# Performance work log

Measured on AMD Instinct MI355X. Metric: run time of the kernel, lower is better.

## Reference

```python
import math
import jax, jax.numpy as jnp
import numpy as np

B, S, D = 32, 2048, 128

def setup_inputs() -> dict:
    key = jax.random.key(0)
    kq, kk, kv, km = jax.random.split(key, 4)
    q = jax.random.normal(kq, (B, S, D), dtype=jnp.float32)
    k = jax.random.normal(kk, (B, S, D), dtype=jnp.float32)
    v = jax.random.normal(kv, (B, S, D), dtype=jnp.float32)
    mask = jax.random.uniform(km, (B, S, S), dtype=jnp.float32)
    return {"q": q, "k": k, "v": v, "mask": mask}

def reference(q, k, v, mask):
    # scaled_product = (q @ k^T) / sqrt(d), then MULTIPLICATIVE mask, softmax, @ v
    scale = 1.0 / math.sqrt(k.shape[-1])
    scores = jnp.einsum("bqd,bkd->bqk", q, k) * scale  # [B, Sq, Sk]
    scores = scores * mask
    weights = jax.nn.softmax(scores, axis=-1)
    return jnp.einsum("bqk,bkd->bqd", weights, v)
```

## Files before the change

### kernel.cpp

```cpp
#include <hip/hip_runtime.h>
#include <math.h>

#define BATCH 32
#define SEQ   2048
#define DH    128
#define QT    64
#define KT    64
#define SCALE 0.08838834764831845f

typedef _Float16 f16;
typedef _Float16 f16x4 __attribute__((ext_vector_type(4)));
typedef _Float16 f16x8 __attribute__((ext_vector_type(8)));
typedef float    f32x4 __attribute__((ext_vector_type(4)));

__device__ __forceinline__ void gld16(const void* g, void* l) {
    __builtin_amdgcn_global_load_lds(
        (const __attribute__((address_space(1))) unsigned int*)g,
        (__attribute__((address_space(3))) unsigned int*)l,
        16, 0, 0);
}

__global__ __launch_bounds__(256)
void cvt_k_kernel(const float* __restrict__ src, f16* __restrict__ dst) {
    size_t i = ((size_t)blockIdx.x * 256 + threadIdx.x) * 8;
    f32x4 a = *(const f32x4*)&src[i];
    f32x4 c = *(const f32x4*)&src[i + 4];
    f16x8 h = { (f16)a.x,(f16)a.y,(f16)a.z,(f16)a.w,(f16)c.x,(f16)c.y,(f16)c.z,(f16)c.w };
    *(f16x8*)&dst[i] = h;
}

__global__ __launch_bounds__(256)
void tr_v_kernel(const float* __restrict__ v, f16* __restrict__ vt) {
    __shared__ f16 t[128 * 80];
    const int tid  = threadIdx.x;
    const int srow = tid >> 5, scol = tid & 31;
    const int b  = blockIdx.x >> 5;
    const int s0 = (blockIdx.x & 31) * 64;
    const size_t base = (size_t)b * SEQ * DH;
    #pragma unroll
    for (int p = 0; p < 8; ++p) {
        int j = p * 8 + srow;
        const float* vr = &v[base + (size_t)(s0 + j) * DH];
        #pragma unroll
        for (int i = 0; i < 4; ++i)
            t[(scol + 32 * i) * 80 + j] = (f16)vr[scol + 32 * i];
    }
    __syncthreads();
    #pragma unroll
    for (int p = 0; p < 4; ++p) {
        int c = p * 256 + tid;
        int d = c >> 3, col = (c & 7) * 8;
        f16x8 h = *(const f16x8*)&t[d * 80 + col];
        *(f16x8*)&vt[(size_t)b * DH * SEQ + (size_t)d * SEQ + s0 + col] = h;
    }
}

__global__ __launch_bounds__(256, 4)
void ScaledDotProductAttention_46720654246409_kernel(
    const float* __restrict__ q, const f16* __restrict__ k16,
    const f16* __restrict__ vt16, const float* __restrict__ mask,
    float* __restrict__ out)
{
    __shared__ f16 ks[64 * 128];
    __shared__ f16 vs[128 * 64];
    __shared__ f16 ps[4 * 16 * 64];

    const int tid  = threadIdx.x;
    const int wv   = tid >> 6;
    const int lane = tid & 63;
    const int quad = lane >> 4;
    const int l16  = lane & 15;
    const int m3   = l16 & 7;
    const int srow = tid >> 5;
    const int scol = tid & 31;

    const int bidx = blockIdx.x;
    const int b    = bidx >> 5;
    const int q0   = (bidx & 31) * QT;

    const size_t qkvBase = (size_t)b * SEQ * DH;
    const size_t mBase   = (size_t)b * SEQ * SEQ;

    char* ksb = (char*)ks;
    char* vsb = (char*)vs;
    char* psb = (char*)ps + wv * 2048;

    #pragma unroll
    for (int p = 0; p < 8; ++p) {
        int r = p * 8 + srow;
        f32x4 x = *(const f32x4*)&q[qkvBase + (size_t)(q0 + r) * DH + scol * 4];
        f16x4 h = { (f16)x.x, (f16)x.y, (f16)x.z, (f16)x.w };
        *(f16x4*)(ksb + r * 256 + ((scol * 8) ^ ((r & 7) << 4))) = h;
    }
    __syncthreads();

    f16x8 aq[4];
    #pragma unroll
    for (int dc = 0; dc < 4; ++dc)
        aq[dc] = *(const f16x8*)(ksb + (wv * 16 + l16) * 256 + ((dc * 64 + quad * 16) ^ (m3 << 4)));
    __syncthreads();

    float m_run = -INFINITY, l_run = 0.f;
    f32x4 o[8];
    #pragma unroll
    for (int f = 0; f < 8; ++f) o[f] = (f32x4){0.f, 0.f, 0.f, 0.f};

    const f16* kbase = k16  + qkvBase;
    const f16* vbase = vt16 + (size_t)b * DH * SEQ;

    #pragma unroll 1
    for (int kt = 0; kt < SEQ / KT; ++kt) {
        const int k0 = kt * KT;

        #pragma unroll
        for (int i = 0; i < 4; ++i) {
            int c   = wv * 4 + i;
            int row = c * 4 + (lane >> 4);
            gld16(kbase + (size_t)(k0 + row) * DH + 8 * ((lane & 15) ^ (row & 7)),
                  ksb + c * 1024);
        }
        #pragma unroll
        for (int i = 0; i < 4; ++i) {
            int c   = wv * 4 + i;
            int row = c * 8 + (lane >> 3);
            gld16(vbase + (size_t)row * SEQ + k0 + 8 * ((lane & 7) ^ (row & 7)),
                  vsb + c * 1024);
        }

        f32x4 mk[4];
        const float* mrow = &mask[mBase + (size_t)(q0 + wv * 16 + l16) * SEQ + k0 + quad * 4];
        #pragma unroll
        for (int f = 0; f < 4; ++f)
            mk[f] = __builtin_nontemporal_load((const f32x4*)(mrow + f * 16));

        __syncthreads();

        f32x4 sc[4];
        #pragma unroll
        for (int f = 0; f < 4; ++f) {
            sc[f] = (f32x4){0.f, 0.f, 0.f, 0.f};
            #pragma unroll
            for (int dc = 0; dc < 4; ++dc) {
                f16x8 kf = *(const f16x8*)(ksb + (f * 16 + l16) * 256 +
                                           ((dc * 64 + quad * 16) ^ (m3 << 4)));
                sc[f] = __builtin_amdgcn_mfma_f32_16x16x32_f16(kf, aq[dc], sc[f], 0, 0, 0);
            }
        }

        float sf[4][4];
        float mx = -INFINITY;
        #pragma unroll
        for (int f = 0; f < 4; ++f)
            #pragma unroll
            for (int r = 0; r < 4; ++r) {
                sf[f][r] = sc[f][r] * SCALE * mk[f][r];
                mx = fmaxf(mx, sf[f][r]);
            }
        mx = fmaxf(mx, __shfl_xor(mx, 16));
        mx = fmaxf(mx, __shfl_xor(mx, 32));
        float mn = fmaxf(m_run, mx);
        float al = __expf(m_run - mn);
        float sum = 0.f;
        float pv[4][4];
        #pragma unroll
        for (int f = 0; f < 4; ++f)
            #pragma unroll
            for (int r = 0; r < 4; ++r) { pv[f][r] = __expf(sf[f][r] - mn); sum += pv[f][r]; }
        sum += __shfl_xor(sum, 16);
        sum += __shfl_xor(sum, 32);
        m_run = mn;
        l_run = l_run * al + sum;
        float alpha[4];
        #pragma unroll
        for (int r = 0; r < 4; ++r) alpha[r] = __shfl(al, quad * 4 + r, 16);

        #pragma unroll
        for (int f = 0; f < 4; ++f) {
            f16x4 pk = { (f16)pv[f][0], (f16)pv[f][1], (f16)pv[f][2], (f16)pv[f][3] };
            *(f16x4*)(psb + l16 * 128 + ((f * 32 + quad * 8) ^ (m3 << 4))) = pk;
        }
        asm volatile("s_waitcnt lgkmcnt(0)" ::: "memory");

        f16x8 ap0 = *(const f16x8*)(psb + l16 * 128 + ((quad * 16) ^ (m3 << 4)));
        f16x8 ap1 = *(const f16x8*)(psb + l16 * 128 + ((64 + quad * 16) ^ (m3 << 4)));

        #pragma unroll
        for (int f = 0; f < 8; ++f) {
            #pragma unroll
            for (int r = 0; r < 4; ++r) o[f][r] *= alpha[r];
            const char* vrow = vsb + (f * 16 + l16) * 128;
            f16x8 bv0 = *(const f16x8*)(vrow + ((quad * 16) ^ (m3 << 4)));
            f16x8 bv1 = *(const f16x8*)(vrow + ((64 + quad * 16) ^ (m3 << 4)));
            o[f] = __builtin_amdgcn_mfma_f32_16x16x32_f16(ap0, bv0, o[f], 0, 0, 0);
            o[f] = __builtin_amdgcn_mfma_f32_16x16x32_f16(ap1, bv1, o[f], 0, 0, 0);
        }
        __syncthreads();
    }

    float linv[4];
    #pragma unroll
    for (int r = 0; r < 4; ++r) linv[r] = 1.0f / __shfl(l_run, quad * 4 + r, 16);
    #pragma unroll
    for (int r = 0; r < 4; ++r)
        #pragma unroll
        for (int f = 0; f < 8; ++f)
            __builtin_nontemporal_store(o[f][r] * linv[r],
                &out[qkvBase + (size_t)(q0 + wv * 16 + quad * 4 + r) * DH + f * 16 + l16]);
}

__global__ __launch_bounds__(256, 3)
void attn_fallback_kernel(
    const float* __restrict__ q, const float* __restrict__ k,
    const float* __restrict__ v, const float* __restrict__ mask,
    float* __restrict__ out)
{
    __shared__ f16 ks[KT * 136];
    __shared__ f16 vs[DH * 72];
    __shared__ f16 ps[4 * 16 * 72];

    const int tid  = threadIdx.x;
    const int wv   = tid >> 6;
    const int lane = tid & 63;
    const int quad = lane >> 4;
    const int l16  = lane & 15;
    const int srow = tid >> 5;
    const int scol = tid & 31;

    const int bidx = blockIdx.x;
    const int b    = bidx >> 5;
    const int q0   = (bidx & 31) * QT;

    const size_t qkvBase = (size_t)b * SEQ * DH;
    const size_t mBase   = (size_t)b * SEQ * SEQ;

    #pragma unroll
    for (int p = 0; p < 8; ++p) {
        int r = p * 8 + srow;
        f32x4 x = *(const f32x4*)&q[qkvBase + (size_t)(q0 + r) * DH + scol * 4];
        f16x4 h = { (f16)x.x, (f16)x.y, (f16)x.z, (f16)x.w };
        *(f16x4*)&ks[r * 136 + scol * 4] = h;
    }
    __syncthreads();

    f16x8 aq[4];
    #pragma unroll
    for (int dc = 0; dc < 4; ++dc)
        aq[dc] = *(const f16x8*)&ks[(wv * 16 + l16) * 136 + dc * 32 + quad * 8];
    __syncthreads();

    float m_run[4] = { -INFINITY, -INFINITY, -INFINITY, -INFINITY };
    float l_run[4] = { 0.f, 0.f, 0.f, 0.f };
    f32x4 o[8];
    #pragma unroll
    for (int f = 0; f < 8; ++f) o[f] = (f32x4){0.f, 0.f, 0.f, 0.f};

    for (int kt = 0; kt < SEQ / KT; ++kt) {
        const int k0 = kt * KT;

        float mk[4][4];
        #pragma unroll
        for (int f = 0; f < 4; ++f)
            #pragma unroll
            for (int r = 0; r < 4; ++r)
                mk[f][r] = mask[mBase + (size_t)(q0 + wv*16 + quad*4 + r) * SEQ
                                + k0 + f*16 + l16];

        #pragma unroll
        for (int p = 0; p < 8; ++p) {
            int r = p * 8 + srow;
            f32x4 x = *(const f32x4*)&k[qkvBase + (size_t)(k0 + r) * DH + scol * 4];
            f16x4 h = { (f16)x.x, (f16)x.y, (f16)x.z, (f16)x.w };
            *(f16x4*)&ks[r * 136 + scol * 4] = h;
        }
        #pragma unroll
        for (int p = 0; p < 8; ++p) {
            int j = p * 8 + srow;
            const float* vr = &v[qkvBase + (size_t)(k0 + j) * DH];
            #pragma unroll
            for (int i = 0; i < 4; ++i)
                vs[(scol + 32*i) * 72 + j] = (f16)vr[scol + 32*i];
        }
        __syncthreads();

        f32x4 sc[4];
        #pragma unroll
        for (int f = 0; f < 4; ++f) {
            sc[f] = (f32x4){0.f, 0.f, 0.f, 0.f};
            #pragma unroll
            for (int dc = 0; dc < 4; ++dc) {
                f16x8 bk = *(const f16x8*)&ks[(f*16 + l16) * 136 + dc*32 + quad*8];
                sc[f] = __builtin_amdgcn_mfma_f32_16x16x32_f16(aq[dc], bk, sc[f], 0, 0, 0);
            }
        }

        float pj[4][4];
        float alpha[4];
        #pragma unroll
        for (int r = 0; r < 4; ++r) {
            float sf[4];
            #pragma unroll
            for (int f = 0; f < 4; ++f) sf[f] = sc[f][r] * SCALE * mk[f][r];
            float mx = fmaxf(fmaxf(sf[0], sf[1]), fmaxf(sf[2], sf[3]));
            #pragma unroll
            for (int off = 1; off < 16; off <<= 1)
                mx = fmaxf(mx, __shfl_xor(mx, off, 16));
            float mn = fmaxf(m_run[r], mx);
            float al = __expf(m_run[r] - mn);
            float sum = 0.f;
            #pragma unroll
            for (int f = 0; f < 4; ++f) { pj[f][r] = __expf(sf[f] - mn); sum += pj[f][r]; }
            #pragma unroll
            for (int off = 1; off < 16; off <<= 1)
                sum += __shfl_xor(sum, off, 16);
            m_run[r] = mn;
            l_run[r] = l_run[r] * al + sum;
            alpha[r] = al;
        }

        #pragma unroll
        for (int f = 0; f < 4; ++f)
            #pragma unroll
            for (int r = 0; r < 4; ++r)
                ps[(wv*16 + quad*4 + r) * 72 + f*16 + l16] = (f16)pj[f][r];
        asm volatile("s_waitcnt lgkmcnt(0)" ::: "memory");

        f16x8 ap0 = *(const f16x8*)&ps[(wv*16 + l16) * 72 + quad*8];
        f16x8 ap1 = *(const f16x8*)&ps[(wv*16 + l16) * 72 + 32 + quad*8];

        #pragma unroll
        for (int f = 0; f < 8; ++f) {
            #pragma unroll
            for (int r = 0; r < 4; ++r) o[f][r] *= alpha[r];
            f16x8 bv0 = *(const f16x8*)&vs[(f*16 + l16) * 72 + quad*8];
            f16x8 bv1 = *(const f16x8*)&vs[(f*16 + l16) * 72 + 32 + quad*8];
            o[f] = __builtin_amdgcn_mfma_f32_16x16x32_f16(ap0, bv0, o[f], 0, 0, 0);
            o[f] = __builtin_amdgcn_mfma_f32_16x16x32_f16(ap1, bv1, o[f], 0, 0, 0);
        }
        __syncthreads();
    }

    #pragma unroll
    for (int r = 0; r < 4; ++r) {
        float inv = 1.0f / l_run[r];
        #pragma unroll
        for (int f = 0; f < 8; ++f)
            out[qkvBase + (size_t)(q0 + wv*16 + quad*4 + r) * DH + f*16 + l16]
                = o[f][r] * inv;
    }
}

extern "C" void kernel_launch(void* const* d_in, const int* in_sizes, int n_in,
                              void* d_out, int out_size, void* d_ws, size_t ws_size,
                              hipStream_t stream) {
    const float* q    = (const float*)d_in[0];
    const float* k    = (const float*)d_in[1];
    const float* v    = (const float*)d_in[2];
    const float* mask = (const float*)d_in[3];
    float* out = (float*)d_out;

    const size_t elems = (size_t)BATCH * SEQ * DH;
    if (d_ws && ws_size >= 2 * elems * sizeof(f16)) {
        f16* k16  = (f16*)d_ws;
        f16* vt16 = k16 + elems;
        hipLaunchKernelGGL(cvt_k_kernel, dim3((unsigned)(elems / 2048)), dim3(256), 0, stream,
                           k, k16);
        hipLaunchKernelGGL(tr_v_kernel, dim3(BATCH * (SEQ / 64)), dim3(256), 0, stream,
                           v, vt16);
        hipLaunchKernelGGL(ScaledDotProductAttention_46720654246409_kernel,
                           dim3(BATCH * (SEQ / QT)), dim3(256), 0, stream,
                           q, k16, vt16, mask, out);
    } else {
        hipLaunchKernelGGL(attn_fallback_kernel,
                           dim3(BATCH * (SEQ / QT)), dim3(256), 0, stream,
                           q, k, v, mask, out);
    }
}
```

Before: 812.0 us.

## Double-buffer K/V tiles and prefetch mask one iteration ahead

Doubles the LDS buffers for K and V and issues the next tile's global-to-LDS loads and mask register loads at the start of the current iteration, so memory latency overlaps the MFMA and softmax work. The loop is unrolled by two to ping-pong between buffers. It also raises wave priority around the MFMA blocks with s_setprio. The larger LDS footprint lowers the launch bound from 4 to 2 blocks per CU, so there is less occupancy to hide latency. The extra mask registers also raise register pressure.

```diff
diff --git a/kernel.cpp b/kernel.cpp
--- a/kernel.cpp
+++ b/kernel.cpp
@@ -55,14 +55,14 @@
     }
 }
 
-__global__ __launch_bounds__(256, 4)
+__global__ __launch_bounds__(256, 2)
 void ScaledDotProductAttention_46720654246409_kernel(
     const float* __restrict__ q, const f16* __restrict__ k16,
     const f16* __restrict__ vt16, const float* __restrict__ mask,
     float* __restrict__ out)
 {
-    __shared__ f16 ks[64 * 128];
-    __shared__ f16 vs[128 * 64];
+    __shared__ f16 ks[2 * 64 * 128];
+    __shared__ f16 vs[2 * 128 * 64];
     __shared__ f16 ps[4 * 16 * 64];
 
     const int tid  = threadIdx.x;
@@ -81,71 +81,87 @@
     const size_t qkvBase = (size_t)b * SEQ * DH;
     const size_t mBase   = (size_t)b * SEQ * SEQ;
 
-    char* ksb = (char*)ks;
-    char* vsb = (char*)vs;
+    char* ks0 = (char*)ks;  char* ks1 = ks0 + 16384;
+    char* vs0 = (char*)vs;  char* vs1 = vs0 + 16384;
     char* psb = (char*)ps + wv * 2048;
+
+    const f16* kbase = k16  + qkvBase;
+    const f16* vbase = vt16 + (size_t)b * DH * SEQ;
+    const float* mptr = mask + mBase + (size_t)(q0 + wv * 16 + l16) * SEQ + quad * 4;
 
     #pragma unroll
     for (int p = 0; p < 8; ++p) {
         int r = p * 8 + srow;
         f32x4 x = *(const f32x4*)&q[qkvBase + (size_t)(q0 + r) * DH + scol * 4];
         f16x4 h = { (f16)x.x, (f16)x.y, (f16)x.z, (f16)x.w };
-        *(f16x4*)(ksb + r * 256 + ((scol * 8) ^ ((r & 7) << 4))) = h;
+        *(f16x4*)(ks0 + r * 256 + ((scol * 8) ^ ((r & 7) << 4))) = h;
     }
     __syncthreads();
 
     f16x8 aq[4];
     #pragma unroll
     for (int dc = 0; dc < 4; ++dc)
-        aq[dc] = *(const f16x8*)(ksb + (wv * 16 + l16) * 256 + ((dc * 64 + quad * 16) ^ (m3 << 4)));
-    __syncthreads();
-
-    float m_run = -INFINITY, l_run = 0.f;
-    f32x4 o[8];
-    #pragma unroll
-    for (int f = 0; f < 8; ++f) o[f] = (f32x4){0.f, 0.f, 0.f, 0.f};
-
-    const f16* kbase = k16  + qkvBase;
-    const f16* vbase = vt16 + (size_t)b * DH * SEQ;
-
-    #pragma unroll 1
-    for (int kt = 0; kt < SEQ / KT; ++kt) {
-        const int k0 = kt * KT;
-
+        aq[dc] = *(const f16x8*)(ks0 + (wv * 16 + l16) * 256 + ((dc * 64 + quad * 16) ^ (m3 << 4)));
+    __syncthreads();
+
+    auto stageK = [&](int kt, char* dst) {
         #pragma unroll
         for (int i = 0; i < 4; ++i) {
             int c   = wv * 4 + i;
             int row = c * 4 + (lane >> 4);
-            gld16(kbase + (size_t)(k0 + row) * DH + 8 * ((lane & 15) ^ (row & 7)),
-                  ksb + c * 1024);
-        }
+            gld16(kbase + (size_t)(kt * KT + row) * DH + 8 * ((lane & 15) ^ (row & 7)),
+                  dst + c * 1024);
+        }
+    };
+    auto stageV = [&](int kt, char* dst) {
         #pragma unroll
         for (int i = 0; i < 4; ++i) {
             int c   = wv * 4 + i;
             int row = c * 8 + (lane >> 3);
-            gld16(vbase + (size_t)row * SEQ + k0 + 8 * ((lane & 7) ^ (row & 7)),
-                  vsb + c * 1024);
-        }
-
-        f32x4 mk[4];
-        const float* mrow = &mask[mBase + (size_t)(q0 + wv * 16 + l16) * SEQ + k0 + quad * 4];
+            gld16(vbase + (size_t)row * SEQ + kt * KT + 8 * ((lane & 7) ^ (row & 7)),
+                  dst + c * 1024);
+        }
+    };
+    auto loadMask = [&](int kt, f32x4 (&mk)[4]) {
+        const float* mr = mptr + kt * KT;
         #pragma unroll
         for (int f = 0; f < 4; ++f)
-            mk[f] = __builtin_nontemporal_load((const f32x4*)(mrow + f * 16));
-
-        __syncthreads();
+            mk[f] = __builtin_nontemporal_load((const f32x4*)(mr + f * 16));
+    };
+
+    float m_run = -INFINITY, l_run = 0.f;
+    f32x4 o[8];
+    #pragma unroll
+    for (int f = 0; f < 8; ++f) o[f] = (f32x4){0.f, 0.f, 0.f, 0.f};
+
+    f32x4 mkA[4], mkB[4];
+
+    loadMask(0, mkA);
+    stageK(0, ks0);
+    stageV(0, vs0);
+    __syncthreads();
+
+    auto body = [&](int kt, char* ksC, char* vsC, char* ksN, char* vsN,
+                    f32x4 (&mkC)[4], f32x4 (&mkN)[4]) {
+        if (kt + 1 < SEQ / KT) {
+            loadMask(kt + 1, mkN);
+            stageK(kt + 1, ksN);
+            stageV(kt + 1, vsN);
+        }
 
         f32x4 sc[4];
+        __builtin_amdgcn_s_setprio(1);
         #pragma unroll
         for (int f = 0; f < 4; ++f) {
             sc[f] = (f32x4){0.f, 0.f, 0.f, 0.f};
             #pragma unroll
             for (int dc = 0; dc < 4; ++dc) {
-                f16x8 kf = *(const f16x8*)(ksb + (f * 16 + l16) * 256 +
+                f16x8 kf = *(const f16x8*)(ksC + (f * 16 + l16) * 256 +
                                            ((dc * 64 + quad * 16) ^ (m3 << 4)));
                 sc[f] = __builtin_amdgcn_mfma_f32_16x16x32_f16(kf, aq[dc], sc[f], 0, 0, 0);
             }
         }
+        __builtin_amdgcn_s_setprio(0);
 
         float sf[4][4];
         float mx = -INFINITY;
@@ -153,7 +169,7 @@
         for (int f = 0; f < 4; ++f)
             #pragma unroll
             for (int r = 0; r < 4; ++r) {
-                sf[f][r] = sc[f][r] * SCALE * mk[f][r];
+                sf[f][r] = sc[f][r] * SCALE * mkC[f][r];
                 mx = fmaxf(mx, sf[f][r]);
             }
         mx = fmaxf(mx, __shfl_xor(mx, 16));
@@ -184,17 +200,26 @@
         f16x8 ap0 = *(const f16x8*)(psb + l16 * 128 + ((quad * 16) ^ (m3 << 4)));
         f16x8 ap1 = *(const f16x8*)(psb + l16 * 128 + ((64 + quad * 16) ^ (m3 << 4)));
 
+        __builtin_amdgcn_s_setprio(1);
         #pragma unroll
         for (int f = 0; f < 8; ++f) {
             #pragma unroll
             for (int r = 0; r < 4; ++r) o[f][r] *= alpha[r];
-            const char* vrow = vsb + (f * 16 + l16) * 128;
+            const char* vrow = vsC + (f * 16 + l16) * 128;
             f16x8 bv0 = *(const f16x8*)(vrow + ((quad * 16) ^ (m3 << 4)));
             f16x8 bv1 = *(const f16x8*)(vrow + ((64 + quad * 16) ^ (m3 << 4)));
             o[f] = __builtin_amdgcn_mfma_f32_16x16x32_f16(ap0, bv0, o[f], 0, 0, 0);
             o[f] = __builtin_amdgcn_mfma_f32_16x16x32_f16(ap1, bv1, o[f], 0, 0, 0);
         }
+        __builtin_amdgcn_s_setprio(0);
+
         __syncthreads();
+    };
+
+    #pragma unroll 1
+    for (int t2 = 0; t2 < (SEQ / KT) / 2; ++t2) {
+        body(2 * t2,     ks0, vs0, ks1, vs1, mkA, mkB);
+        body(2 * t2 + 1, ks1, vs1, ks0, vs0, mkB, mkA);
     }
 
     float linv[4];
```

Result: no change. 820.3 us (+1.0%).
